# Performance work log

Measured on AMD Instinct MI355X. Metric: run time of the kernel, lower is better.

The kernel has to match this reference:

```python
import jax, jax.numpy as jnp
import numpy as np

DIM = 3072
NUM_HEADS = 24
HEAD_DIM = 128
INNER = NUM_HEADS * HEAD_DIM
EPS = 1e-5


def _layernorm(x, eps=EPS):
    # affine-free LayerNorm over the last (head_dim) axis
    mu = jnp.mean(x, axis=-1, keepdims=True)
    var = jnp.mean(jnp.square(x - mu), axis=-1, keepdims=True)
    return (x - mu) * jax.lax.rsqrt(var + eps)


def _rope_interleaved(x, cos, sin):
    # x: (B, S_img, H, D); cos/sin: (S_img, D//2). Non-neox (interleaved) style.
    x1 = x[..., 0::2]
    x2 = x[..., 1::2]
    c = cos[None, :, None, :]
    s = sin[None, :, None, :]
    o1 = x1 * c - x2 * s
    o2 = x2 * c + x1 * s
    return jnp.stack([o1, o2], axis=-1).reshape(x.shape)


def setup_inputs() -> dict:
    key = jax.random.key(0)
    ks = jax.random.split(key, 8)
    B, S_txt, S_img = 1, 256, 2048
    hidden_states = jax.random.normal(ks[0], (B, S_img, DIM), dtype=jnp.float32)
    encoder_hidden_states = jax.random.normal(ks[1], (B, S_txt, DIM), dtype=jnp.float32)
    cos = jax.random.uniform(ks[2], (S_img, HEAD_DIM // 2), dtype=jnp.float32)
    sin = jax.random.uniform(ks[3], (S_img, HEAD_DIM // 2), dtype=jnp.float32)
    Wqkv = jax.random.normal(ks[4], (DIM, 3 * INNER), dtype=jnp.float32) * (DIM ** -0.5)
    bqkv = jnp.zeros((3 * INNER,), dtype=jnp.float32)
    Wout = jax.random.normal(ks[5], (INNER, DIM), dtype=jnp.float32) * (INNER ** -0.5)
    bout = jnp.zeros((DIM,), dtype=jnp.float32)
    return {
        "hidden_states": hidden_states,
        "encoder_hidden_states": encoder_hidden_states,
        "cos": cos,
        "sin": sin,
        "Wqkv": Wqkv,
        "bqkv": bqkv,
        "Wout": Wout,
        "bout": bout,
        "text_seq_length": 256,
    }


def reference(hidden_states, encoder_hidden_states, cos, sin, Wqkv, bqkv, Wout, bout, text_seq_length):
    T = text_seq_length
    x = jnp.concatenate([encoder_hidden_states, hidden_states], axis=1)  # (B, S, dim)
    B, S, _ = x.shape
    qkv = x @ Wqkv + bqkv  # (B, S, 3*inner)
    q, k, v = jnp.split(qkv, 3, axis=-1)
    q = q.reshape(B, S, NUM_HEADS, HEAD_DIM)
    k = k.reshape(B, S, NUM_HEADS, HEAD_DIM)
    v = v.reshape(B, S, NUM_HEADS, HEAD_DIM)
    q = _layernorm(q)
    k = _layernorm(k)
    # partial RoPE: only on image-token slice
    q = jnp.concatenate([q[:, :T], _rope_interleaved(q[:, T:], cos, sin)], axis=1)
    k = jnp.concatenate([k[:, :T], _rope_interleaved(k[:, T:], cos, sin)], axis=1)
    scale = 1.0 / (HEAD_DIM ** 0.5)
    scores = jnp.einsum("bqhd,bkhd->bhqk", q, k) * scale
    probs = jax.nn.softmax(scores, axis=-1)
    out = jnp.einsum("bhqk,bkhd->bqhd", probs, v)
    out = out.reshape(B, S, INNER)
    out = out @ Wout + bout
    encoder_out = out[:, :T, :]
    hidden_out = out[:, T:, :]
    return (hidden_out, encoder_out)
```

## Files before the change

kernel.cpp:

```cpp
#include <hip/hip_runtime.h>

#define DIMC 3072
#define NH 24
#define HD 128
#define QKV_N 9216
#define S_TXT 256
#define S_IMG 2048
#define S_TOT 2304

typedef _Float16 f16x8 __attribute__((ext_vector_type(8)));
typedef _Float16 f16x4 __attribute__((ext_vector_type(4)));
typedef _Float16 f16x2 __attribute__((ext_vector_type(2)));
typedef float f32x4 __attribute__((ext_vector_type(4)));

#define MFMA(A, B, C) __builtin_amdgcn_mfma_f32_16x16x32_f16(A, B, C, 0, 0, 0)

#define QSCALE (0.08838834764831845f * 1.4426950408889634f)

__device__ __forceinline__ void gl2lds16(const _Float16* g, _Float16* l) {
    __builtin_amdgcn_global_load_lds(
        (const __attribute__((address_space(1))) unsigned int*)g,
        (__attribute__((address_space(3))) unsigned int*)l,
        16, 0, 0);
}

__global__ __launch_bounds__(256) void split_x(
    const float* __restrict__ enc, const float* __restrict__ hid,
    _Float16* __restrict__ xh)
{
    const int s = blockIdx.x;
    const float* src = (s < S_TXT) ? enc + (size_t)s * DIMC
                                   : hid + (size_t)(s - S_TXT) * DIMC;
    const int t = threadIdx.x;
#pragma unroll
    for (int it = 0; it < 3; ++it) {
        const int i = (it * 256 + t) * 4;
        float4 v = *(const float4*)(src + i);
        f16x4 hv;
        hv.x = (_Float16)v.x; hv.y = (_Float16)v.y;
        hv.z = (_Float16)v.z; hv.w = (_Float16)v.w;
        *(f16x4*)(xh + (size_t)s * DIMC + i) = hv;
    }
}

__global__ __launch_bounds__(256) void transpose_w_hi(
    const float* __restrict__ W, const int ldw, _Float16* __restrict__ Th)
{
    __shared__ float T[64][68];
    const int n0 = blockIdx.x * 64, k0 = blockIdx.y * 64;
    const int t = threadIdx.x;
    {
        const int r = t >> 2, c4 = (t & 3) * 16;
#pragma unroll
        for (int j = 0; j < 4; ++j) {
            float4 v = *(const float4*)(W + (size_t)(k0 + r) * ldw + n0 + c4 + j * 4);
            *(float4*)&T[r][c4 + j * 4] = v;
        }
    }
    __syncthreads();
    const int nr = t >> 2, kp = (t & 3) * 16;
    f16x8 hv0, hv1;
#pragma unroll
    for (int j = 0; j < 8; ++j) hv0[j] = (_Float16)T[kp + j][nr];
#pragma unroll
    for (int j = 0; j < 8; ++j) hv1[j] = (_Float16)T[kp + 8 + j][nr];
    _Float16* dh = Th + (size_t)(n0 + nr) * DIMC + k0 + kp;
    *(f16x8*)(dh) = hv0; *(f16x8*)(dh + 8) = hv1;
}

__global__ __launch_bounds__(256) void gemm_qkv(
    const _Float16* __restrict__ Ah, const _Float16* __restrict__ Bh,
    const float* __restrict__ bias,
    _Float16* __restrict__ Qh, _Float16* __restrict__ Kh,
    _Float16* __restrict__ Vt)
{
    __shared__ __attribute__((aligned(16))) _Float16 Ash[128 * 32];
    __shared__ __attribute__((aligned(16))) _Float16 Bsh[128 * 32];

    const int cpx = (int)gridDim.x >> 3;
    const int wgid = (blockIdx.x & 7) * cpx + (blockIdx.x >> 3);
    const int bm = (wgid % 18) * 128;
    const int bn = (wgid / 18) * 128;

    const int tid = threadIdx.x;
    const int l = tid & 63, w = tid >> 6;
    const int wr = w >> 1, wc = w & 1;
    const int lr = l & 15, g = l >> 4;

    const int srow0 = w * 32 + (l >> 2);
    const int srow1 = srow0 + 16;
    const int skp0 = (((l & 3) ^ ((srow0 >> 1) & 3)) * 8);
    const int skp1 = (((l & 3) ^ ((srow1 >> 1) & 3)) * 8);
    const _Float16* gA0 = Ah + (size_t)(bm + srow0) * DIMC + skp0;
    const _Float16* gA1 = Ah + (size_t)(bm + srow1) * DIMC + skp1;
    const _Float16* gB0 = Bh + (size_t)(bn + srow0) * DIMC + skp0;
    const _Float16* gB1 = Bh + (size_t)(bn + srow1) * DIMC + skp1;
    _Float16* lA0 = &Ash[(w * 32) * 32];
    _Float16* lA1 = &Ash[(w * 32 + 16) * 32];
    _Float16* lB0 = &Bsh[(w * 32) * 32];
    _Float16* lB1 = &Bsh[(w * 32 + 16) * 32];

    int aoff[4], boff[4];
#pragma unroll
    for (int i = 0; i < 4; ++i) {
        const int ra = wr * 64 + i * 16 + lr;
        const int rb = wc * 64 + i * 16 + lr;
        aoff[i] = ra * 32 + ((g ^ ((ra >> 1) & 3)) * 8);
        boff[i] = rb * 32 + ((g ^ ((rb >> 1) & 3)) * 8);
    }

    f32x4 acc[4][4] = {};

    for (int k0 = 0; k0 < DIMC; k0 += 32) {
        gl2lds16(gA0 + k0, lA0);
        gl2lds16(gA1 + k0, lA1);
        gl2lds16(gB0 + k0, lB0);
        gl2lds16(gB1 + k0, lB1);
        __syncthreads();

        f16x8 bhf[4];
#pragma unroll
        for (int ni = 0; ni < 4; ++ni)
            bhf[ni] = *(const f16x8*)&Bsh[boff[ni]];
#pragma unroll
        for (int mi = 0; mi < 4; ++mi) {
            f16x8 ahf = *(const f16x8*)&Ash[aoff[mi]];
#pragma unroll
            for (int ni = 0; ni < 4; ++ni)
                acc[mi][ni] = MFMA(ahf, bhf[ni], acc[mi][ni]);
        }
        __syncthreads();
    }

    const int nb = bn >> 7;
    const int typ = nb / NH;
    const int h = nb % NH;

    if (typ == 2) {
#pragma unroll
        for (int mi = 0; mi < 4; ++mi) {
            const int sbase = bm + wr * 64 + mi * 16 + g * 4;
#pragma unroll
            for (int ni = 0; ni < 4; ++ni) {
                const int col = wc * 64 + ni * 16 + lr;
                const float bv = bias[bn + col];
                f16x4 vv;
                vv.x = (_Float16)(acc[mi][ni][0] + bv);
                vv.y = (_Float16)(acc[mi][ni][1] + bv);
                vv.z = (_Float16)(acc[mi][ni][2] + bv);
                vv.w = (_Float16)(acc[mi][ni][3] + bv);
                *(f16x4*)&Vt[((size_t)h * HD + col) * S_TOT + sbase] = vv;
            }
        }
    } else {
        _Float16* dst = (typ ? Kh : Qh) + (size_t)h * S_TOT * HD;
#pragma unroll
        for (int mi = 0; mi < 4; ++mi)
#pragma unroll
            for (int ni = 0; ni < 4; ++ni) {
                const int col = wc * 64 + ni * 16 + lr;
                const float bv = bias[bn + col];
#pragma unroll
                for (int e = 0; e < 4; ++e) {
                    const int r = bm + wr * 64 + mi * 16 + g * 4 + e;
                    dst[(size_t)r * HD + col] = (_Float16)(acc[mi][ni][e] + bv);
                }
            }
    }
}

template <int REMAP>
__global__ __launch_bounds__(256) void gemm_f16_lds(
    const _Float16* __restrict__ Ah, const _Float16* __restrict__ Bh,
    const float* __restrict__ bias, float* __restrict__ C,
    const int nblk_m, const int ldc)
{
    __shared__ __attribute__((aligned(16))) _Float16 Ash[128 * 32];
    __shared__ __attribute__((aligned(16))) _Float16 Bsh[128 * 32];

    const int cpx = (int)gridDim.x >> 3;
    const int wgid = (blockIdx.x & 7) * cpx + (blockIdx.x >> 3);
    const int bm = (wgid % nblk_m) * 128;
    const int bn = (wgid / nblk_m) * 128;

    const int tid = threadIdx.x;
    const int l = tid & 63, w = tid >> 6;
    const int wr = w >> 1, wc = w & 1;
    const int lr = l & 15, g = l >> 4;

    const int srow0 = w * 32 + (l >> 2);
    const int srow1 = srow0 + 16;
    const int skp0 = (((l & 3) ^ ((srow0 >> 1) & 3)) * 8);
    const int skp1 = (((l & 3) ^ ((srow1 >> 1) & 3)) * 8);
    const _Float16* gA0 = Ah + (size_t)(bm + srow0) * DIMC + skp0;
    const _Float16* gA1 = Ah + (size_t)(bm + srow1) * DIMC + skp1;
    const _Float16* gB0 = Bh + (size_t)(bn + srow0) * DIMC + skp0;
    const _Float16* gB1 = Bh + (size_t)(bn + srow1) * DIMC + skp1;
    _Float16* lA0 = &Ash[(w * 32) * 32];
    _Float16* lA1 = &Ash[(w * 32 + 16) * 32];
    _Float16* lB0 = &Bsh[(w * 32) * 32];
    _Float16* lB1 = &Bsh[(w * 32 + 16) * 32];

    int aoff[4], boff[4];
#pragma unroll
    for (int i = 0; i < 4; ++i) {
        const int ra = wr * 64 + i * 16 + lr;
        const int rb = wc * 64 + i * 16 + lr;
        aoff[i] = ra * 32 + ((g ^ ((ra >> 1) & 3)) * 8);
        boff[i] = rb * 32 + ((g ^ ((rb >> 1) & 3)) * 8);
    }

    f32x4 acc[4][4] = {};

    for (int k0 = 0; k0 < DIMC; k0 += 32) {
        gl2lds16(gA0 + k0, lA0);
        gl2lds16(gA1 + k0, lA1);
        gl2lds16(gB0 + k0, lB0);
        gl2lds16(gB1 + k0, lB1);
        __syncthreads();

        f16x8 bhf[4];
#pragma unroll
        for (int ni = 0; ni < 4; ++ni)
            bhf[ni] = *(const f16x8*)&Bsh[boff[ni]];
#pragma unroll
        for (int mi = 0; mi < 4; ++mi) {
            f16x8 ahf = *(const f16x8*)&Ash[aoff[mi]];
#pragma unroll
            for (int ni = 0; ni < 4; ++ni)
                acc[mi][ni] = MFMA(ahf, bhf[ni], acc[mi][ni]);
        }
        __syncthreads();
    }

#pragma unroll
    for (int mi = 0; mi < 4; ++mi)
#pragma unroll
        for (int ni = 0; ni < 4; ++ni) {
            const int cl = bn + wc * 64 + ni * 16 + lr;
            const float bv = bias[cl];
#pragma unroll
            for (int e = 0; e < 4; ++e) {
                const int r = bm + wr * 64 + mi * 16 + g * 4 + e;
                if (REMAP) {
                    const int gr = (r < S_TXT) ? (S_IMG + r) : (r - S_TXT);
                    C[(size_t)gr * DIMC + cl] = acc[mi][ni][e] + bv;
                } else {
                    C[(size_t)r * ldc + cl] = acc[mi][ni][e] + bv;
                }
            }
        }
}

__global__ __launch_bounds__(256) void ln_rope_inplace(
    _Float16* __restrict__ Qh, _Float16* __restrict__ Kh,
    const float* __restrict__ cost, const float* __restrict__ sint)
{
    const int wave = threadIdx.x >> 6;
    const int lane = threadIdx.x & 63;
    const int task = blockIdx.x * 4 + wave;
    const int s = task / 48;
    const int rem = task % 48;
    const int qk = rem / 24;
    const int h = rem % 24;

    _Float16* p = (qk ? Kh : Qh) + ((size_t)h * S_TOT + s) * HD + lane * 2;
    f16x2 xv = *(const f16x2*)p;
    float x0 = (float)xv.x, x1 = (float)xv.y;

    float sum = x0 + x1;
    float sq = x0 * x0 + x1 * x1;
#pragma unroll
    for (int off = 1; off < 64; off <<= 1) {
        sum += __shfl_xor(sum, off, 64);
        sq  += __shfl_xor(sq, off, 64);
    }
    const float mu = sum * (1.0f / 128.0f);
    const float var = sq * (1.0f / 128.0f) - mu * mu;
    const float rstd = rsqrtf(var + 1e-5f);
    float y0 = (x0 - mu) * rstd;
    float y1 = (x1 - mu) * rstd;

    if (s >= S_TXT) {
        const int ip = s - S_TXT;
        const float c = cost[ip * 64 + lane];
        const float sn = sint[ip * 64 + lane];
        const float o0 = y0 * c - y1 * sn;
        const float o1 = y1 * c + y0 * sn;
        y0 = o0; y1 = o1;
    }
    if (qk == 0) { y0 *= QSCALE; y1 *= QSCALE; }

    f16x2 hv; hv.x = (_Float16)y0; hv.y = (_Float16)y1;
    *(f16x2*)p = hv;
}

__global__ __launch_bounds__(512) void attn_mfma(
    const _Float16* __restrict__ Qg, const _Float16* __restrict__ Kg,
    const _Float16* __restrict__ Vg, _Float16* __restrict__ aoh)
{
    __shared__ __attribute__((aligned(16))) _Float16 Ksh[4 * 64 * 32];
    __shared__ __attribute__((aligned(16))) _Float16 Vsh[128 * 64];
    __shared__ __attribute__((aligned(16))) _Float16 Pah[8 * 16 * 64];

    const int wgid = ((int)blockIdx.x & 7) * 54 + ((int)blockIdx.x >> 3);
    const int h = wgid / 18;
    const int q0 = (wgid % 18) * 128;
    const int tid = threadIdx.x;
    const int w = tid >> 6, l = tid & 63;
    const int lr = l & 15, g = l >> 4;

    const int qrow = q0 + w * 16 + lr;
    const _Float16* qb = Qg + ((size_t)h * S_TOT + qrow) * HD + g * 8;
    f16x8 qh[4];
#pragma unroll
    for (int db = 0; db < 4; ++db)
        qh[db] = *(const f16x8*)(qb + db * 32);

    f32x4 o[8] = {};
    float mrow = -3.0e38f, lrow = 0.0f;

    const int kxr = (lr >> 1) & 3;
    const int px  = lr & 7;
    int ksl[4];
#pragma unroll
    for (int db = 0; db < 4; ++db) ksl[db] = (g ^ kxr ^ db) * 8;
    const int vs0 = (g ^ px) * 8;
    const int vs1 = ((4 + g) ^ px) * 8;

    const int kkv = tid >> 3, kd = tid & 7;
    const int kdb = kd >> 1, kg0 = (kd & 1) * 2;
    const int kx = (kkv >> 1) & 3;
    const int kbase = kdb * 2048 + kkv * 32;
    const int vd = tid >> 2, vh = tid & 3;
    const int vx = vd & 7;
    const int vbase = vd * 64;
    const int vg0 = vh * 2;
    const _Float16* gK = Kg + ((size_t)h * S_TOT + kkv) * HD + kd * 16;
    const _Float16* gV = Vg + ((size_t)h * HD + vd) * S_TOT + vh * 16;

    uint4 rK0, rK1, rV0, rV1;
#define LOADKV(kv0) { \
    rK0 = *(const uint4*)(gK + (size_t)(kv0) * HD);     rK1 = *(const uint4*)(gK + (size_t)(kv0) * HD + 8); \
    rV0 = *(const uint4*)(gV + (kv0));                  rV1 = *(const uint4*)(gV + (kv0) + 8); }

    LOADKV(0);

    for (int kb = 0; kb < S_TOT / 64; ++kb) {
        __syncthreads();
        *(uint4*)&Ksh[kbase + (((kg0 + 0) ^ kx ^ kdb) * 8)] = rK0;
        *(uint4*)&Ksh[kbase + (((kg0 + 1) ^ kx ^ kdb) * 8)] = rK1;
        *(uint4*)&Vsh[vbase + (((vg0 + 0) ^ vx) * 8)] = rV0;
        *(uint4*)&Vsh[vbase + (((vg0 + 1) ^ vx) * 8)] = rV1;
        __syncthreads();
        if (kb + 1 < S_TOT / 64) LOADKV((kb + 1) * 64);

        f32x4 sT[4] = {};
        __builtin_amdgcn_s_setprio(1);
#pragma unroll
        for (int db = 0; db < 4; ++db)
#pragma unroll
            for (int mf = 0; mf < 4; ++mf) {
                f16x8 kf = *(const f16x8*)&Ksh[db * 2048 + (mf * 16 + lr) * 32 + ksl[db]];
                sT[mf] = MFMA(kf, qh[db], sT[mf]);
            }
        __builtin_amdgcn_s_setprio(0);

        float pm = -3.0e38f;
#pragma unroll
        for (int mf = 0; mf < 4; ++mf)
#pragma unroll
            for (int e = 0; e < 4; ++e)
                pm = fmaxf(pm, sT[mf][e]);
        pm = fmaxf(pm, __shfl_xor(pm, 16, 64));
        pm = fmaxf(pm, __shfl_xor(pm, 32, 64));

        if (__any(pm > mrow + 11.0f)) {
            const float mnew = fmaxf(mrow, pm);
            const float alpha = exp2f(mrow - mnew);
            lrow *= alpha;
            mrow = mnew;
            const float a0 = __shfl(alpha, g * 4 + 0, 64);
            const float a1 = __shfl(alpha, g * 4 + 1, 64);
            const float a2 = __shfl(alpha, g * 4 + 2, 64);
            const float a3 = __shfl(alpha, g * 4 + 3, 64);
#pragma unroll
            for (int df = 0; df < 8; ++df) {
                o[df][0] *= a0; o[df][1] *= a1; o[df][2] *= a2; o[df][3] *= a3;
            }
        }

        float rs = 0.0f;
        float ex_[4][4];
#pragma unroll
        for (int mf = 0; mf < 4; ++mf)
#pragma unroll
            for (int e = 0; e < 4; ++e) {
                const float pv = exp2f(sT[mf][e] - mrow);
                ex_[mf][e] = pv;
                rs += pv;
            }
        rs += __shfl_xor(rs, 16, 64);
        rs += __shfl_xor(rs, 32, 64);
        lrow += rs;

        {
            const int pbase = w * 1024 + lr * 64;
#pragma unroll
            for (int mf = 0; mf < 4; ++mf) {
                const int slot = ((mf * 2 + (g >> 1)) ^ px) * 8 + (g & 1) * 4;
                f16x2 t0; t0.x = (_Float16)ex_[mf][0]; t0.y = (_Float16)ex_[mf][1];
                f16x2 t1; t1.x = (_Float16)ex_[mf][2]; t1.y = (_Float16)ex_[mf][3];
                *(f16x2*)&Pah[pbase + slot]     = t0;
                *(f16x2*)&Pah[pbase + slot + 2] = t1;
            }
        }

        f16x8 pa0 = *(const f16x8*)&Pah[w * 1024 + lr * 64 + vs0];
        f16x8 pa1 = *(const f16x8*)&Pah[w * 1024 + lr * 64 + vs1];
        __builtin_amdgcn_s_setprio(1);
#pragma unroll
        for (int df = 0; df < 8; ++df) {
            f16x8 vf0 = *(const f16x8*)&Vsh[(df * 16 + lr) * 64 + vs0];
            f16x8 vf1 = *(const f16x8*)&Vsh[(df * 16 + lr) * 64 + vs1];
            o[df] = MFMA(pa0, vf0, o[df]);
            o[df] = MFMA(pa1, vf1, o[df]);
        }
        __builtin_amdgcn_s_setprio(0);
    }
#undef LOADKV

    const float inv = 1.0f / lrow;
    const float b0 = __shfl(inv, g * 4 + 0, 64);
    const float b1 = __shfl(inv, g * 4 + 1, 64);
    const float b2 = __shfl(inv, g * 4 + 2, 64);
    const float b3 = __shfl(inv, g * 4 + 3, 64);
    const float bb[4] = {b0, b1, b2, b3};
#pragma unroll
    for (int df = 0; df < 8; ++df)
#pragma unroll
        for (int e = 0; e < 4; ++e) {
            const int r = q0 + w * 16 + g * 4 + e;
            aoh[(size_t)r * DIMC + h * HD + df * 16 + lr] = (_Float16)(o[df][e] * bb[e]);
        }
}

extern "C" void kernel_launch(void* const* d_in, const int* in_sizes, int n_in,
                              void* d_out, int out_size, void* d_ws, size_t ws_size,
                              hipStream_t stream)
{
    const float* hid  = (const float*)d_in[0];
    const float* enc  = (const float*)d_in[1];
    const float* cost = (const float*)d_in[2];
    const float* sint = (const float*)d_in[3];
    const float* Wqkv = (const float*)d_in[4];
    const float* bqkv = (const float*)d_in[5];
    const float* Wout = (const float*)d_in[6];
    const float* bout = (const float*)d_in[7];
    float* out = (float*)d_out;

    char* ws = (char*)d_ws;
    _Float16* Qh  = (_Float16*)(ws + 0);
    _Float16* Kh  = (_Float16*)(ws + 14155776);
    _Float16* Vth = (_Float16*)(ws + 28311552);
    _Float16* aoh = (_Float16*)(ws + 42467328);
    _Float16* xh  = (_Float16*)(ws + 56623104);
    _Float16* Wth = (_Float16*)(ws + 70778880);
    _Float16* W2h = (_Float16*)(ws + 127401984);

    split_x<<<S_TOT, 256, 0, stream>>>(enc, hid, xh);
    transpose_w_hi<<<dim3(144, 48), 256, 0, stream>>>(Wqkv, QKV_N, Wth);
    gemm_qkv<<<18 * 72, 256, 0, stream>>>(xh, Wth, bqkv, Qh, Kh, Vth);
    transpose_w_hi<<<dim3(48, 48), 256, 0, stream>>>(Wout, DIMC, W2h);
    ln_rope_inplace<<<(S_TOT * 48) / 4, 256, 0, stream>>>(Qh, Kh, cost, sint);
    attn_mfma<<<432, 512, 0, stream>>>(Qh, Kh, Vth, aoh);
    gemm_f16_lds<1><<<18 * 24, 256, 0, stream>>>(aoh, W2h, bout, out, 18, DIMC);
}
```

Before: 399.7 us.

## Fuse prep kernels and double-buffer LDS in both GEMMs with MFMA priority

Merges the input fp16 conversion and both weight transposes into a single prep launch. Both GEMMs now use two LDS buffers, issuing the next K-tile's global-to-LDS loads before the MFMAs on the current tile so memory latency overlaps compute, and they raise wave priority around the MFMA block. The row mapping for staging loads is also reorganized. In exchange LDS per block doubles, which may lower occupancy.

```diff
diff --git a/kernel.cpp b/kernel.cpp
--- a/kernel.cpp
+++ b/kernel.cpp
@@ -24,31 +24,44 @@
         16, 0, 0);
 }
 
-__global__ __launch_bounds__(256) void split_x(
+__global__ __launch_bounds__(256) void prep(
     const float* __restrict__ enc, const float* __restrict__ hid,
-    _Float16* __restrict__ xh)
-{
-    const int s = blockIdx.x;
-    const float* src = (s < S_TXT) ? enc + (size_t)s * DIMC
-                                   : hid + (size_t)(s - S_TXT) * DIMC;
+    const float* __restrict__ Wqkv, const float* __restrict__ Wout,
+    _Float16* __restrict__ xh, _Float16* __restrict__ Wth,
+    _Float16* __restrict__ W2h)
+{
+    __shared__ float T[64][68];
+    const int bid = blockIdx.x;
     const int t = threadIdx.x;
-#pragma unroll
-    for (int it = 0; it < 3; ++it) {
-        const int i = (it * 256 + t) * 4;
-        float4 v = *(const float4*)(src + i);
-        f16x4 hv;
-        hv.x = (_Float16)v.x; hv.y = (_Float16)v.y;
-        hv.z = (_Float16)v.z; hv.w = (_Float16)v.w;
-        *(f16x4*)(xh + (size_t)s * DIMC + i) = hv;
-    }
-}
-
-__global__ __launch_bounds__(256) void transpose_w_hi(
-    const float* __restrict__ W, const int ldw, _Float16* __restrict__ Th)
-{
-    __shared__ float T[64][68];
-    const int n0 = blockIdx.x * 64, k0 = blockIdx.y * 64;
-    const int t = threadIdx.x;
+
+    if (bid < S_TOT) {
+        const int s = bid;
+        const float* src = (s < S_TXT) ? enc + (size_t)s * DIMC
+                                       : hid + (size_t)(s - S_TXT) * DIMC;
+#pragma unroll
+        for (int it = 0; it < 3; ++it) {
+            const int i = (it * 256 + t) * 4;
+            float4 v = *(const float4*)(src + i);
+            f16x4 hv;
+            hv.x = (_Float16)v.x; hv.y = (_Float16)v.y;
+            hv.z = (_Float16)v.z; hv.w = (_Float16)v.w;
+            *(f16x4*)(xh + (size_t)s * DIMC + i) = hv;
+        }
+        return;
+    }
+
+    const float* W;
+    _Float16* Th;
+    int n0, k0, ldw;
+    if (bid < S_TOT + 144 * 48) {
+        const int b2 = bid - S_TOT;
+        W = Wqkv; Th = Wth; ldw = QKV_N;
+        n0 = (b2 % 144) * 64; k0 = (b2 / 144) * 64;
+    } else {
+        const int b2 = bid - S_TOT - 144 * 48;
+        W = Wout; Th = W2h; ldw = DIMC;
+        n0 = (b2 % 48) * 64; k0 = (b2 / 48) * 64;
+    }
     {
         const int r = t >> 2, c4 = (t & 3) * 16;
 #pragma unroll
@@ -67,6 +80,60 @@
     _Float16* dh = Th + (size_t)(n0 + nr) * DIMC + k0 + kp;
     *(f16x8*)(dh) = hv0; *(f16x8*)(dh + 8) = hv1;
 }
+
+#define GEMM_DB_PRE()                                                         \
+    const int cpx = (int)gridDim.x >> 3;                                      \
+    const int wgid = (blockIdx.x & 7) * cpx + (blockIdx.x >> 3);              \
+    const int bm = (wgid % 18) * 128;                                         \
+    const int bn = (wgid / 18) * 128;                                         \
+    const int tid = threadIdx.x;                                              \
+    const int l = tid & 63, w = tid >> 6;                                     \
+    const int wr = w >> 1, wc = w & 1;                                        \
+    const int lr = l & 15, g = l >> 4;                                        \
+    const int row0 = w * 16 + (l >> 2);                                       \
+    const int swz = (((l & 3) ^ ((row0 >> 1) & 3)) * 8);                      \
+    const _Float16* gA0 = Ah + (size_t)(bm + row0) * DIMC + swz;              \
+    const _Float16* gA1 = Ah + (size_t)(bm + 64 + row0) * DIMC + swz;         \
+    const _Float16* gB0 = Bh + (size_t)(bn + row0) * DIMC + swz;              \
+    const _Float16* gB1 = Bh + (size_t)(bn + 64 + row0) * DIMC + swz;         \
+    int aoff[4], boff[4];                                                     \
+    _Pragma("unroll")                                                         \
+    for (int i = 0; i < 4; ++i) {                                             \
+        const int ra = wr * 64 + i * 16 + lr;                                 \
+        const int rb = wc * 64 + i * 16 + lr;                                 \
+        aoff[i] = ra * 32 + ((g ^ ((ra >> 1) & 3)) * 8);                      \
+        boff[i] = rb * 32 + ((g ^ ((rb >> 1) & 3)) * 8);                      \
+    }
+
+#define GEMM_STAGE(dd, k0) do {                                               \
+    gl2lds16(gA0 + (k0), &Ash[dd][(w * 16) * 32]);                            \
+    gl2lds16(gA1 + (k0), &Ash[dd][(64 + w * 16) * 32]);                       \
+    gl2lds16(gB0 + (k0), &Bsh[dd][(w * 16) * 32]);                            \
+    gl2lds16(gB1 + (k0), &Bsh[dd][(64 + w * 16) * 32]);                       \
+} while (0)
+
+#define GEMM_DB_LOOP()                                                        \
+    f32x4 acc[4][4] = {};                                                     \
+    GEMM_STAGE(0, 0);                                                         \
+    __syncthreads();                                                          \
+    for (int T = 0; T < DIMC / 32; ++T) {                                     \
+        const int d = T & 1;                                                  \
+        if (T + 1 < DIMC / 32) GEMM_STAGE(d ^ 1, (T + 1) * 32);               \
+        f16x8 bhf[4];                                                         \
+        _Pragma("unroll")                                                     \
+        for (int ni = 0; ni < 4; ++ni)                                        \
+            bhf[ni] = *(const f16x8*)&Bsh[d][boff[ni]];                       \
+        __builtin_amdgcn_s_setprio(1);                                        \
+        _Pragma("unroll")                                                     \
+        for (int mi = 0; mi < 4; ++mi) {                                      \
+            f16x8 ahf = *(const f16x8*)&Ash[d][aoff[mi]];                     \
+            _Pragma("unroll")                                                 \
+            for (int ni = 0; ni < 4; ++ni)                                    \
+                acc[mi][ni] = MFMA(ahf, bhf[ni], acc[mi][ni]);                \
+        }                                                                     \
+        __builtin_amdgcn_s_setprio(0);                                        \
+        __syncthreads();                                                      \
+    }
 
 __global__ __launch_bounds__(256) void gemm_qkv(
     const _Float16* __restrict__ Ah, const _Float16* __restrict__ Bh,
@@ -74,63 +141,10 @@
     _Float16* __restrict__ Qh, _Float16* __restrict__ Kh,
     _Float16* __restrict__ Vt)
 {
-    __shared__ __attribute__((aligned(16))) _Float16 Ash[128 * 32];
-    __shared__ __attribute__((aligned(16))) _Float16 Bsh[128 * 32];
-
-    const int cpx = (int)gridDim.x >> 3;
-    const int wgid = (blockIdx.x & 7) * cpx + (blockIdx.x >> 3);
-    const int bm = (wgid % 18) * 128;
-    const int bn = (wgid / 18) * 128;
-
-    const int tid = threadIdx.x;
-    const int l = tid & 63, w = tid >> 6;
-    const int wr = w >> 1, wc = w & 1;
-    const int lr = l & 15, g = l >> 4;
-
-    const int srow0 = w * 32 + (l >> 2);
-    const int srow1 = srow0 + 16;
-    const int skp0 = (((l & 3) ^ ((srow0 >> 1) & 3)) * 8);
-    const int skp1 = (((l & 3) ^ ((srow1 >> 1) & 3)) * 8);
-    const _Float16* gA0 = Ah + (size_t)(bm + srow0) * DIMC + skp0;
-    const _Float16* gA1 = Ah + (size_t)(bm + srow1) * DIMC + skp1;
-    const _Float16* gB0 = Bh + (size_t)(bn + srow0) * DIMC + skp0;
-    const _Float16* gB1 = Bh + (size_t)(bn + srow1) * DIMC + skp1;
-    _Float16* lA0 = &Ash[(w * 32) * 32];
-    _Float16* lA1 = &Ash[(w * 32 + 16) * 32];
-    _Float16* lB0 = &Bsh[(w * 32) * 32];
-    _Float16* lB1 = &Bsh[(w * 32 + 16) * 32];
-
-    int aoff[4], boff[4];
-#pragma unroll
-    for (int i = 0; i < 4; ++i) {
-        const int ra = wr * 64 + i * 16 + lr;
-        const int rb = wc * 64 + i * 16 + lr;
-        aoff[i] = ra * 32 + ((g ^ ((ra >> 1) & 3)) * 8);
-        boff[i] = rb * 32 + ((g ^ ((rb >> 1) & 3)) * 8);
-    }
-
-    f32x4 acc[4][4] = {};
-
-    for (int k0 = 0; k0 < DIMC; k0 += 32) {
-        gl2lds16(gA0 + k0, lA0);
-        gl2lds16(gA1 + k0, lA1);
-        gl2lds16(gB0 + k0, lB0);
-        gl2lds16(gB1 + k0, lB1);
-        __syncthreads();
-
-        f16x8 bhf[4];
-#pragma unroll
-        for (int ni = 0; ni < 4; ++ni)
-            bhf[ni] = *(const f16x8*)&Bsh[boff[ni]];
-#pragma unroll
-        for (int mi = 0; mi < 4; ++mi) {
-            f16x8 ahf = *(const f16x8*)&Ash[aoff[mi]];
-#pragma unroll
-            for (int ni = 0; ni < 4; ++ni)
-                acc[mi][ni] = MFMA(ahf, bhf[ni], acc[mi][ni]);
-        }
-        __syncthreads();
-    }
+    __shared__ __attribute__((aligned(16))) _Float16 Ash[2][128 * 32];
+    __shared__ __attribute__((aligned(16))) _Float16 Bsh[2][128 * 32];
+    GEMM_DB_PRE()
+    GEMM_DB_LOOP()
 
     const int nb = bn >> 7;
     const int typ = nb / NH;
@@ -169,69 +183,14 @@
     }
 }
 
-template <int REMAP>
-__global__ __launch_bounds__(256) void gemm_f16_lds(
+__global__ __launch_bounds__(256) void gemm_out(
     const _Float16* __restrict__ Ah, const _Float16* __restrict__ Bh,
-    const float* __restrict__ bias, float* __restrict__ C,
-    const int nblk_m, const int ldc)
-{
-    __shared__ __attribute__((aligned(16))) _Float16 Ash[128 * 32];
-    __shared__ __attribute__((aligned(16))) _Float16 Bsh[128 * 32];
-
-    const int cpx = (int)gridDim.x >> 3;
-    const int wgid = (blockIdx.x & 7) * cpx + (blockIdx.x >> 3);
-    const int bm = (wgid % nblk_m) * 128;
-    const int bn = (wgid / nblk_m) * 128;
-
-    const int tid = threadIdx.x;
-    const int l = tid & 63, w = tid >> 6;
-    const int wr = w >> 1, wc = w & 1;
-    const int lr = l & 15, g = l >> 4;
-
-    const int srow0 = w * 32 + (l >> 2);
-    const int srow1 = srow0 + 16;
-    const int skp0 = (((l & 3) ^ ((srow0 >> 1) & 3)) * 8);
-    const int skp1 = (((l & 3) ^ ((srow1 >> 1) & 3)) * 8);
-    const _Float16* gA0 = Ah + (size_t)(bm + srow0) * DIMC + skp0;
-    const _Float16* gA1 = Ah + (size_t)(bm + srow1) * DIMC + skp1;
-    const _Float16* gB0 = Bh + (size_t)(bn + srow0) * DIMC + skp0;
-    const _Float16* gB1 = Bh + (size_t)(bn + srow1) * DIMC + skp1;
-    _Float16* lA0 = &Ash[(w * 32) * 32];
-    _Float16* lA1 = &Ash[(w * 32 + 16) * 32];
-    _Float16* lB0 = &Bsh[(w * 32) * 32];
-    _Float16* lB1 = &Bsh[(w * 32 + 16) * 32];
-
-    int aoff[4], boff[4];
-#pragma unroll
-    for (int i = 0; i < 4; ++i) {
-        const int ra = wr * 64 + i * 16 + lr;
-        const int rb = wc * 64 + i * 16 + lr;
-        aoff[i] = ra * 32 + ((g ^ ((ra >> 1) & 3)) * 8);
-        boff[i] = rb * 32 + ((g ^ ((rb >> 1) & 3)) * 8);
-    }
-
-    f32x4 acc[4][4] = {};
-
-    for (int k0 = 0; k0 < DIMC; k0 += 32) {
-        gl2lds16(gA0 + k0, lA0);
-        gl2lds16(gA1 + k0, lA1);
-        gl2lds16(gB0 + k0, lB0);
-        gl2lds16(gB1 + k0, lB1);
-        __syncthreads();
-
-        f16x8 bhf[4];
-#pragma unroll
-        for (int ni = 0; ni < 4; ++ni)
-            bhf[ni] = *(const f16x8*)&Bsh[boff[ni]];
-#pragma unroll
-        for (int mi = 0; mi < 4; ++mi) {
-            f16x8 ahf = *(const f16x8*)&Ash[aoff[mi]];
-#pragma unroll
-            for (int ni = 0; ni < 4; ++ni)
-                acc[mi][ni] = MFMA(ahf, bhf[ni], acc[mi][ni]);
-        }
-        __syncthreads();
-    }
+    const float* __restrict__ bias, float* __restrict__ C)
+{
+    __shared__ __attribute__((aligned(16))) _Float16 Ash[2][128 * 32];
+    __shared__ __attribute__((aligned(16))) _Float16 Bsh[2][128 * 32];
+    GEMM_DB_PRE()
+    GEMM_DB_LOOP()
 
 #pragma unroll
     for (int mi = 0; mi < 4; ++mi)
@@ -242,12 +201,8 @@
 #pragma unroll
             for (int e = 0; e < 4; ++e) {
                 const int r = bm + wr * 64 + mi * 16 + g * 4 + e;
-                if (REMAP) {
-                    const int gr = (r < S_TXT) ? (S_IMG + r) : (r - S_TXT);
-                    C[(size_t)gr * DIMC + cl] = acc[mi][ni][e] + bv;
-                } else {
-                    C[(size_t)r * ldc + cl] = acc[mi][ni][e] + bv;
-                }
+                const int gr = (r < S_TXT) ? (S_IMG + r) : (r - S_TXT);
+                C[(size_t)gr * DIMC + cl] = acc[mi][ni][e] + bv;
             }
         }
 }
@@ -468,11 +423,10 @@
     _Float16* Wth = (_Float16*)(ws + 70778880);
     _Float16* W2h = (_Float16*)(ws + 127401984);
 
-    split_x<<<S_TOT, 256, 0, stream>>>(enc, hid, xh);
-    transpose_w_hi<<<dim3(144, 48), 256, 0, stream>>>(Wqkv, QKV_N, Wth);
+    prep<<<S_TOT + 144 * 48 + 48 * 48, 256, 0, stream>>>(
+        enc, hid, Wqkv, Wout, xh, Wth, W2h);
     gemm_qkv<<<18 * 72, 256, 0, stream>>>(xh, Wth, bqkv, Qh, Kh, Vth);
-    transpose_w_hi<<<dim3(48, 48), 256, 0, stream>>>(Wout, DIMC, W2h);
     ln_rope_inplace<<<(S_TOT * 48) / 4, 256, 0, stream>>>(Qh, Kh, cost, sint);
     attn_mfma<<<432, 512, 0, stream>>>(Qh, Kh, Vth, aoh);
-    gemm_f16_lds<1><<<18 * 24, 256, 0, stream>>>(aoh, W2h, bout, out, 18, DIMC);
-}
+    gemm_out<<<18 * 24, 256, 0, stream>>>(aoh, W2h, bout, out);
+}
```

New measurement: 457.4 us. +14.4%, slower.
